# Kernel optimization log

Measured on AMD Instinct MI355X. Metric: run time of the kernel, lower is better.

Reference implementation:

```python
import jax, jax.numpy as jnp
import numpy as np
import math

B, T, F, H = 8, 1024, 1024, 16
D = F // H

def setup_inputs() -> dict:
    key = jax.random.key(0)
    ks = jax.random.split(key, 6)
    s = 1.0 / math.sqrt(F)
    return {
        "qkv": jax.random.normal(ks[0], (B, T, F), dtype=jnp.float32),
        "key_padding_mask": jax.random.randint(ks[1], (B, T), 0, 2).astype(bool),
        "in_proj_w": jax.random.normal(ks[2], (3 * F, F), dtype=jnp.float32) * s,
        "in_proj_b": jax.random.normal(ks[3], (3 * F,), dtype=jnp.float32) * 0.02,
        "out_proj_w": jax.random.normal(ks[4], (F, F), dtype=jnp.float32) * s,
        "out_proj_b": jax.random.normal(ks[5], (F,), dtype=jnp.float32) * 0.02,
    }

def reference(qkv, key_padding_mask, in_proj_w, in_proj_b, out_proj_w, out_proj_b):
    b, t, f = qkv.shape
    h, d = H, f // H
    norm = jnp.asarray(math.sqrt(d), dtype=qkv.dtype)
    # fused QKV projection (torch Linear: x @ W.T + b)
    x = qkv @ in_proj_w.T + in_proj_b                     # [B, T, 3F]
    q, k, v = jnp.split(x, 3, axis=-1)
    q = q.reshape(b, t, h, d).transpose(0, 2, 1, 3)       # [B, H, T, D]
    k = k.reshape(b, t, h, d).transpose(0, 2, 1, 3)
    v = v.reshape(b, t, h, d).transpose(0, 2, 1, 3)
    dot = jnp.einsum("bhqd,bhkd->bhqk", q, k) / norm      # [B, H, T, T]
    dot = jnp.where(key_padding_mask[:, None, None, :], -jnp.inf, dot)
    alpha = jax.nn.softmax(dot, axis=-1)                  # [B, H, T, T]
    att = jnp.einsum("bhqk,bhkd->bhqd", alpha, v)         # [B, H, T, D]
    att = att.transpose(0, 2, 1, 3).reshape(b, t, f)      # [B, T, F]
    out = att @ out_proj_w.T + out_proj_b
    return (out, alpha)
```

## Files before the change

### kernel.cpp

```cpp
#include <hip/hip_runtime.h>
#include <math.h>

#define B_ 8
#define T_ 1024
#define F_ 1024
#define H_ 16
#define D_ 64

typedef __bf16 bf16x8 __attribute__((ext_vector_type(8)));
typedef float f32x4 __attribute__((ext_vector_type(4)));
typedef unsigned short u16x8 __attribute__((ext_vector_type(8)));

__device__ __forceinline__ unsigned short f2bf(float f) {
    union { float f; unsigned u; } v; v.f = f;
    unsigned r = v.u + 0x7fffu + ((v.u >> 16) & 1u);
    return (unsigned short)(r >> 16);
}

__device__ __forceinline__ void gld16(const void* g, void* l) {
    __builtin_amdgcn_global_load_lds(
        (const __attribute__((address_space(1))) void*)g,
        (__attribute__((address_space(3))) void*)l, 16, 0, 0);
}

__device__ __forceinline__ int swz4(int row15) {
    return (row15 ^ (row15 >> 2)) & 3;
}

__global__ __launch_bounds__(256) void cvt_f32_bf16(
    const float* __restrict__ in, unsigned short* __restrict__ out, int n8)
{
    int i = blockIdx.x * 256 + threadIdx.x;
    if (i >= n8) return;
    const float4* p = (const float4*)in + (size_t)i * 2;
    float4 x = p[0], y = p[1];
    u16x8 o;
    o[0] = f2bf(x.x); o[1] = f2bf(x.y); o[2] = f2bf(x.z); o[3] = f2bf(x.w);
    o[4] = f2bf(y.x); o[5] = f2bf(y.y); o[6] = f2bf(y.z); o[7] = f2bf(y.w);
    ((u16x8*)out)[i] = o;
}

__global__ __launch_bounds__(256) void qkv_gemm(
    const unsigned short* __restrict__ A,
    const unsigned short* __restrict__ Bw,
    const float* __restrict__ bias,
    unsigned short* __restrict__ qb,
    unsigned short* __restrict__ kb,
    unsigned short* __restrict__ vb)
{
    __shared__ __align__(16) unsigned short As[128 * 32];
    __shared__ __align__(16) unsigned short Bs[128 * 32];
    const int K = 1024;
    int tid = threadIdx.x;
    int lane = tid & 63, wave = tid >> 6;
    int wr = wave >> 1, wc = wave & 1;
    int m0 = blockIdx.y * 128, n0 = blockIdx.x * 128;
    int col = lane & 15, quad = lane >> 4;
    int sw = swz4(col);
    int rl = lane >> 2;
    int lc = (lane & 3) ^ swz4(rl);

    f32x4 acc[4][4] = {};
    for (int kc = 0; kc < K; kc += 32) {
        __syncthreads();
        #pragma unroll
        for (int l = 0; l < 2; l++) {
            int ia = wave * 2 + l;
            gld16(A  + (size_t)(m0 + ia * 16 + rl) * K + kc + lc * 8, &As[ia * 512]);
            gld16(Bw + (size_t)(n0 + ia * 16 + rl) * K + kc + lc * 8, &Bs[ia * 512]);
        }
        __syncthreads();
        bf16x8 af[4], bg[4];
        #pragma unroll
        for (int mt = 0; mt < 4; mt++)
            af[mt] = *(const bf16x8*)&As[(wr * 64 + mt * 16 + col) * 32 + ((quad ^ sw)) * 8];
        #pragma unroll
        for (int nt = 0; nt < 4; nt++)
            bg[nt] = *(const bf16x8*)&Bs[(wc * 64 + nt * 16 + col) * 32 + ((quad ^ sw)) * 8];
        #pragma unroll
        for (int mt = 0; mt < 4; mt++)
            #pragma unroll
            for (int nt = 0; nt < 4; nt++)
                acc[mt][nt] = __builtin_amdgcn_mfma_f32_16x16x32_bf16(
                    af[mt], bg[nt], acc[mt][nt], 0, 0, 0);
    }
    int which = n0 >> 10;
    #pragma unroll
    for (int nt = 0; nt < 4; nt++) {
        int n = n0 + wc * 64 + nt * 16 + col;
        int hn = (n & 1023) >> 6, d = n & 63;
        float bn = bias[n];
        #pragma unroll
        for (int mt = 0; mt < 4; mt++) {
            #pragma unroll
            for (int r = 0; r < 4; r++) {
                int m = m0 + wr * 64 + mt * 16 + quad * 4 + r;
                int bb = m >> 10, t = m & 1023;
                unsigned short bf = f2bf(acc[mt][nt][r] + bn);
                if (which == 0)
                    qb[(size_t)((bb * H_ + hn) * T_ + t) * D_ + d] = bf;
                else if (which == 1)
                    kb[(size_t)((bb * H_ + hn) * T_ + t) * D_ + d] = bf;
                else
                    vb[(size_t)((bb * H_ + hn) * D_ + d) * T_ + t] = bf;
            }
        }
    }
}

__global__ __launch_bounds__(256) void attn_kernel(
    const unsigned short* __restrict__ qb,
    const unsigned short* __restrict__ kb,
    const int* __restrict__ mask,
    float* __restrict__ alpha)
{
    __shared__ __align__(16) unsigned short Qs[16 * 72];
    __shared__ __align__(16) unsigned short Ks[4][64 * 64];
    __shared__ float redmax[4][16];
    __shared__ float redsum[4][16];
    int b = blockIdx.z, h = blockIdx.y, q0 = blockIdx.x * 16;
    int tid = threadIdx.x, lane = tid & 63, wave = tid >> 6;
    int col = lane & 15, quad = lane >> 4;
    const unsigned short* qbase = qb + ((size_t)(b * H_ + h) * T_ + q0) * D_;
    const unsigned short* kbase = kb + ((size_t)(b * H_ + h) * T_) * D_;

    if (tid < 128) {
        int r = tid >> 3, c = tid & 7;
        *(u16x8*)&Qs[r * 72 + c * 8] = *(const u16x8*)&qbase[r * 64 + c * 8];
    }
    int krl = lane >> 3;
    int klc = (lane & 7) ^ krl;
    int sw8 = col & 7;
    f32x4 acc[4][4] = {};
    bf16x8 aq0, aq1;
    for (int it = 0; it < 4; it++) {
        int kr0 = wave * 256 + it * 64;
        #pragma unroll
        for (int j = 0; j < 8; j++)
            gld16(kbase + (size_t)(kr0 + j * 8 + krl) * 64 + klc * 8, &Ks[wave][j * 512]);
        __syncthreads();
        if (it == 0) {
            aq0 = *(const bf16x8*)&Qs[col * 72 + quad * 8];
            aq1 = *(const bf16x8*)&Qs[col * 72 + 32 + quad * 8];
        }
        #pragma unroll
        for (int ct = 0; ct < 4; ct++) {
            int r = ct * 16 + col;
            const unsigned short* kp = &Ks[wave][r * 64];
            bf16x8 b0 = *(const bf16x8*)&kp[(quad ^ sw8) * 8];
            bf16x8 b1 = *(const bf16x8*)&kp[((4 + quad) ^ sw8) * 8];
            acc[it][ct] = __builtin_amdgcn_mfma_f32_16x16x32_bf16(aq0, b0, acc[it][ct], 0, 0, 0);
            acc[it][ct] = __builtin_amdgcn_mfma_f32_16x16x32_bf16(aq1, b1, acc[it][ct], 0, 0, 0);
        }
        __syncthreads();
    }
    const int* mrow = mask + b * T_;
    float mx[4] = {-INFINITY, -INFINITY, -INFINITY, -INFINITY};
    #pragma unroll
    for (int it = 0; it < 4; it++)
        #pragma unroll
        for (int ct = 0; ct < 4; ct++) {
            int k = wave * 256 + it * 64 + ct * 16 + col;
            bool m = mrow[k] != 0;
            #pragma unroll
            for (int r = 0; r < 4; r++) {
                float v = m ? -INFINITY : acc[it][ct][r] * 0.125f;
                acc[it][ct][r] = v;
                mx[r] = fmaxf(mx[r], v);
            }
        }
    #pragma unroll
    for (int r = 0; r < 4; r++) {
        mx[r] = fmaxf(mx[r], __shfl_xor(mx[r], 1, 64));
        mx[r] = fmaxf(mx[r], __shfl_xor(mx[r], 2, 64));
        mx[r] = fmaxf(mx[r], __shfl_xor(mx[r], 4, 64));
        mx[r] = fmaxf(mx[r], __shfl_xor(mx[r], 8, 64));
    }
    if (col == 0)
        #pragma unroll
        for (int r = 0; r < 4; r++) redmax[wave][quad * 4 + r] = mx[r];
    __syncthreads();
    float gm[4];
    #pragma unroll
    for (int r = 0; r < 4; r++) {
        int row = quad * 4 + r;
        gm[r] = fmaxf(fmaxf(redmax[0][row], redmax[1][row]),
                      fmaxf(redmax[2][row], redmax[3][row]));
    }
    float sm[4] = {0.f, 0.f, 0.f, 0.f};
    #pragma unroll
    for (int it = 0; it < 4; it++)
        #pragma unroll
        for (int ct = 0; ct < 4; ct++)
            #pragma unroll
            for (int r = 0; r < 4; r++) {
                float e = __expf(acc[it][ct][r] - gm[r]);
                acc[it][ct][r] = e;
                sm[r] += e;
            }
    #pragma unroll
    for (int r = 0; r < 4; r++) {
        sm[r] += __shfl_xor(sm[r], 1, 64);
        sm[r] += __shfl_xor(sm[r], 2, 64);
        sm[r] += __shfl_xor(sm[r], 4, 64);
        sm[r] += __shfl_xor(sm[r], 8, 64);
    }
    if (col == 0)
        #pragma unroll
        for (int r = 0; r < 4; r++) redsum[wave][quad * 4 + r] = sm[r];
    __syncthreads();
    float inv[4];
    #pragma unroll
    for (int r = 0; r < 4; r++) {
        int row = quad * 4 + r;
        inv[r] = 1.0f / (redsum[0][row] + redsum[1][row] + redsum[2][row] + redsum[3][row]);
    }
    float* abase = alpha + ((size_t)(b * H_ + h) * T_ + q0) * T_;
    #pragma unroll
    for (int it = 0; it < 4; it++)
        #pragma unroll
        for (int ct = 0; ct < 4; ct++) {
            int k = wave * 256 + it * 64 + ct * 16 + col;
            #pragma unroll
            for (int r = 0; r < 4; r++)
                abase[(size_t)(quad * 4 + r) * T_ + k] = acc[it][ct][r] * inv[r];
        }
}

__global__ __launch_bounds__(256) void attn_v_kernel(
    const float* __restrict__ alpha,
    const unsigned short* __restrict__ vb,
    unsigned short* __restrict__ attb)
{
    __shared__ __align__(16) unsigned short As[64 * 72];
    __shared__ __align__(16) unsigned short Vs[64 * 32];
    int b = blockIdx.z, h = blockIdx.y, q0 = blockIdx.x * 64;
    int tid = threadIdx.x, lane = tid & 63, wave = tid >> 6;
    int col = lane & 15, quad = lane >> 4;
    int swv = swz4(col);
    const float* abase = alpha + ((size_t)(b * H_ + h) * T_ + q0) * T_;
    const unsigned short* vbase = vb + (size_t)(b * H_ + h) * D_ * T_;
    int ar = tid >> 2, acg = tid & 3;
    int vrl = lane >> 2;
    int vlc = (lane & 3) ^ swz4(vrl);
    f32x4 acc[4] = {};
    for (int kc = 0; kc < T_; kc += 32) {
        __syncthreads();
        gld16(vbase + (size_t)(wave * 16 + vrl) * T_ + kc + vlc * 8, &Vs[wave * 512]);
        float4 x = *(const float4*)&abase[(size_t)ar * T_ + kc + acg * 8];
        float4 y = *(const float4*)&abase[(size_t)ar * T_ + kc + acg * 8 + 4];
        u16x8 p;
        p[0] = f2bf(x.x); p[1] = f2bf(x.y); p[2] = f2bf(x.z); p[3] = f2bf(x.w);
        p[4] = f2bf(y.x); p[5] = f2bf(y.y); p[6] = f2bf(y.z); p[7] = f2bf(y.w);
        *(u16x8*)&As[ar * 72 + acg * 8] = p;
        __syncthreads();
        bf16x8 af = *(const bf16x8*)&As[(wave * 16 + col) * 72 + quad * 8];
        #pragma unroll
        for (int nt = 0; nt < 4; nt++) {
            int r = nt * 16 + col;
            bf16x8 bv = *(const bf16x8*)&Vs[r * 32 + ((quad ^ swv)) * 8];
            acc[nt] = __builtin_amdgcn_mfma_f32_16x16x32_bf16(af, bv, acc[nt], 0, 0, 0);
        }
    }
    #pragma unroll
    for (int nt = 0; nt < 4; nt++) {
        int d = nt * 16 + col;
        #pragma unroll
        for (int r = 0; r < 4; r++) {
            int t = q0 + wave * 16 + quad * 4 + r;
            attb[(size_t)(b * T_ + t) * F_ + h * D_ + d] = f2bf(acc[nt][r]);
        }
    }
}

__global__ __launch_bounds__(256) void out_gemm(
    const unsigned short* __restrict__ A,
    const unsigned short* __restrict__ Bw,
    const float* __restrict__ bias,
    float* __restrict__ out)
{
    __shared__ __align__(16) unsigned short As[128 * 32];
    __shared__ __align__(16) unsigned short Bs[128 * 32];
    const int K = 1024;
    int tid = threadIdx.x;
    int lane = tid & 63, wave = tid >> 6;
    int wr = wave >> 1, wc = wave & 1;
    int m0 = blockIdx.y * 128, n0 = blockIdx.x * 128;
    int col = lane & 15, quad = lane >> 4;
    int sw = swz4(col);
    int rl = lane >> 2;
    int lc = (lane & 3) ^ swz4(rl);
    f32x4 acc[4][4] = {};
    for (int kc = 0; kc < K; kc += 32) {
        __syncthreads();
        #pragma unroll
        for (int l = 0; l < 2; l++) {
            int ia = wave * 2 + l;
            gld16(A  + (size_t)(m0 + ia * 16 + rl) * K + kc + lc * 8, &As[ia * 512]);
            gld16(Bw + (size_t)(n0 + ia * 16 + rl) * K + kc + lc * 8, &Bs[ia * 512]);
        }
        __syncthreads();
        bf16x8 af[4], bg[4];
        #pragma unroll
        for (int mt = 0; mt < 4; mt++)
            af[mt] = *(const bf16x8*)&As[(wr * 64 + mt * 16 + col) * 32 + ((quad ^ sw)) * 8];
        #pragma unroll
        for (int nt = 0; nt < 4; nt++)
            bg[nt] = *(const bf16x8*)&Bs[(wc * 64 + nt * 16 + col) * 32 + ((quad ^ sw)) * 8];
        #pragma unroll
        for (int mt = 0; mt < 4; mt++)
            #pragma unroll
            for (int nt = 0; nt < 4; nt++)
                acc[mt][nt] = __builtin_amdgcn_mfma_f32_16x16x32_bf16(
                    af[mt], bg[nt], acc[mt][nt], 0, 0, 0);
    }
    #pragma unroll
    for (int nt = 0; nt < 4; nt++) {
        int n = n0 + wc * 64 + nt * 16 + col;
        float bn = bias[n];
        #pragma unroll
        for (int mt = 0; mt < 4; mt++) {
            #pragma unroll
            for (int r = 0; r < 4; r++) {
                int m = m0 + wr * 64 + mt * 16 + quad * 4 + r;
                out[(size_t)m * F_ + n] = acc[mt][nt][r] + bn;
            }
        }
    }
}

extern "C" void kernel_launch(void* const* d_in, const int* in_sizes, int n_in,
                              void* d_out, int out_size, void* d_ws, size_t ws_size,
                              hipStream_t stream)
{
    const float* qkv   = (const float*)d_in[0];
    const int*   mask  = (const int*)d_in[1];
    const float* in_w  = (const float*)d_in[2];
    const float* in_b  = (const float*)d_in[3];
    const float* out_w = (const float*)d_in[4];
    const float* out_b = (const float*)d_in[5];
    float* out = (float*)d_out;
    const size_t NE = (size_t)B_ * T_ * F_;
    float* alpha = out + NE;

    unsigned short* ws   = (unsigned short*)d_ws;
    unsigned short* Xb   = ws;
    unsigned short* Wib  = Xb  + NE;
    unsigned short* Wob  = Wib + 3 * F_ * F_;
    unsigned short* qb2  = Wob + (size_t)F_ * F_;
    unsigned short* kb2  = qb2 + NE;
    unsigned short* vb2  = kb2 + NE;
    unsigned short* attb = vb2 + NE;

    cvt_f32_bf16<<<dim3((int)(NE / 8 / 256)), 256, 0, stream>>>(qkv, Xb, (int)(NE / 8));
    cvt_f32_bf16<<<dim3(3 * F_ * F_ / 8 / 256), 256, 0, stream>>>(in_w, Wib, 3 * F_ * F_ / 8);
    cvt_f32_bf16<<<dim3(F_ * F_ / 8 / 256), 256, 0, stream>>>(out_w, Wob, F_ * F_ / 8);

    qkv_gemm<<<dim3(24, 64), 256, 0, stream>>>(Xb, Wib, in_b, qb2, kb2, vb2);
    attn_kernel<<<dim3(64, H_, B_), 256, 0, stream>>>(qb2, kb2, mask, alpha);
    attn_v_kernel<<<dim3(16, H_, B_), 256, 0, stream>>>(alpha, vb2, attb);
    out_gemm<<<dim3(8, 64), 256, 0, stream>>>(attb, Wob, out_b, out);
}
```

Baseline: 963.0 us.

## Fuse softmax-probability times V into attention kernel to avoid re-reading alpha

Merges the attention-score/softmax kernel with the alpha·V kernel. Normalized probabilities are kept as bf16 in shared memory, in a buffer that reuses the K staging area, and multiplied by V tiles inside the same block. This removes the second kernel's re-read of the 512MB fp32 alpha tensor from global memory. In exchange it raises LDS usage per block, which may reduce occupancy, and each block now streams all of V for its head instead of sharing V across 64 query rows.

```diff
diff --git a/kernel.cpp b/kernel.cpp
--- a/kernel.cpp
+++ b/kernel.cpp
@@ -108,14 +108,17 @@
     }
 }
 
-__global__ __launch_bounds__(256) void attn_kernel(
+__global__ __launch_bounds__(256) void fused_attn(
     const unsigned short* __restrict__ qb,
     const unsigned short* __restrict__ kb,
+    const unsigned short* __restrict__ vb,
     const int* __restrict__ mask,
-    float* __restrict__ alpha)
-{
+    float* __restrict__ alpha,
+    unsigned short* __restrict__ attb)
+{
+    __shared__ __align__(16) unsigned short U[16 * 1032];
+    __shared__ __align__(16) unsigned short Vs[4][2048];
     __shared__ __align__(16) unsigned short Qs[16 * 72];
-    __shared__ __align__(16) unsigned short Ks[4][64 * 64];
     __shared__ float redmax[4][16];
     __shared__ float redsum[4][16];
     int b = blockIdx.z, h = blockIdx.y, q0 = blockIdx.x * 16;
@@ -123,6 +126,7 @@
     int col = lane & 15, quad = lane >> 4;
     const unsigned short* qbase = qb + ((size_t)(b * H_ + h) * T_ + q0) * D_;
     const unsigned short* kbase = kb + ((size_t)(b * H_ + h) * T_) * D_;
+    unsigned short* Ksw = &U[wave * 4096];
 
     if (tid < 128) {
         int r = tid >> 3, c = tid & 7;
@@ -137,7 +141,7 @@
         int kr0 = wave * 256 + it * 64;
         #pragma unroll
         for (int j = 0; j < 8; j++)
-            gld16(kbase + (size_t)(kr0 + j * 8 + krl) * 64 + klc * 8, &Ks[wave][j * 512]);
+            gld16(kbase + (size_t)(kr0 + j * 8 + krl) * 64 + klc * 8, &Ksw[j * 512]);
         __syncthreads();
         if (it == 0) {
             aq0 = *(const bf16x8*)&Qs[col * 72 + quad * 8];
@@ -146,7 +150,7 @@
         #pragma unroll
         for (int ct = 0; ct < 4; ct++) {
             int r = ct * 16 + col;
-            const unsigned short* kp = &Ks[wave][r * 64];
+            const unsigned short* kp = &Ksw[r * 64];
             bf16x8 b0 = *(const bf16x8*)&kp[(quad ^ sw8) * 8];
             bf16x8 b1 = *(const bf16x8*)&kp[((4 + quad) ^ sw8) * 8];
             acc[it][ct] = __builtin_amdgcn_mfma_f32_16x16x32_bf16(aq0, b0, acc[it][ct], 0, 0, 0);
@@ -222,54 +226,37 @@
         for (int ct = 0; ct < 4; ct++) {
             int k = wave * 256 + it * 64 + ct * 16 + col;
             #pragma unroll
-            for (int r = 0; r < 4; r++)
-                abase[(size_t)(quad * 4 + r) * T_ + k] = acc[it][ct][r] * inv[r];
-        }
-}
-
-__global__ __launch_bounds__(256) void attn_v_kernel(
-    const float* __restrict__ alpha,
-    const unsigned short* __restrict__ vb,
-    unsigned short* __restrict__ attb)
-{
-    __shared__ __align__(16) unsigned short As[64 * 72];
-    __shared__ __align__(16) unsigned short Vs[64 * 32];
-    int b = blockIdx.z, h = blockIdx.y, q0 = blockIdx.x * 64;
-    int tid = threadIdx.x, lane = tid & 63, wave = tid >> 6;
-    int col = lane & 15, quad = lane >> 4;
-    int swv = swz4(col);
-    const float* abase = alpha + ((size_t)(b * H_ + h) * T_ + q0) * T_;
-    const unsigned short* vbase = vb + (size_t)(b * H_ + h) * D_ * T_;
-    int ar = tid >> 2, acg = tid & 3;
-    int vrl = lane >> 2;
-    int vlc = (lane & 3) ^ swz4(vrl);
-    f32x4 acc[4] = {};
-    for (int kc = 0; kc < T_; kc += 32) {
-        __syncthreads();
-        gld16(vbase + (size_t)(wave * 16 + vrl) * T_ + kc + vlc * 8, &Vs[wave * 512]);
-        float4 x = *(const float4*)&abase[(size_t)ar * T_ + kc + acg * 8];
-        float4 y = *(const float4*)&abase[(size_t)ar * T_ + kc + acg * 8 + 4];
-        u16x8 p;
-        p[0] = f2bf(x.x); p[1] = f2bf(x.y); p[2] = f2bf(x.z); p[3] = f2bf(x.w);
-        p[4] = f2bf(y.x); p[5] = f2bf(y.y); p[6] = f2bf(y.z); p[7] = f2bf(y.w);
-        *(u16x8*)&As[ar * 72 + acg * 8] = p;
-        __syncthreads();
-        bf16x8 af = *(const bf16x8*)&As[(wave * 16 + col) * 72 + quad * 8];
-        #pragma unroll
-        for (int nt = 0; nt < 4; nt++) {
-            int r = nt * 16 + col;
-            bf16x8 bv = *(const bf16x8*)&Vs[r * 32 + ((quad ^ swv)) * 8];
-            acc[nt] = __builtin_amdgcn_mfma_f32_16x16x32_bf16(af, bv, acc[nt], 0, 0, 0);
-        }
-    }
-    #pragma unroll
-    for (int nt = 0; nt < 4; nt++) {
-        int d = nt * 16 + col;
-        #pragma unroll
-        for (int r = 0; r < 4; r++) {
-            int t = q0 + wave * 16 + quad * 4 + r;
-            attb[(size_t)(b * T_ + t) * F_ + h * D_ + d] = f2bf(acc[nt][r]);
-        }
+            for (int r = 0; r < 4; r++) {
+                float v = acc[it][ct][r] * inv[r];
+                abase[(size_t)(quad * 4 + r) * T_ + k] = v;
+                U[(quad * 4 + r) * 1032 + k] = f2bf(v);
+            }
+        }
+    __syncthreads();
+    const unsigned short* vhead = vb + (size_t)(b * H_ + h) * D_ * T_;
+    f32x4 oacc = {};
+    for (int kc = 0; kc < T_; kc += 128) {
+        asm volatile("s_waitcnt lgkmcnt(0)" ::: "memory");
+        __builtin_amdgcn_sched_barrier(0);
+        #pragma unroll
+        for (int i = 0; i < 4; i++) {
+            int r = i * 4 + quad;
+            gld16(vhead + (size_t)(wave * 16 + r) * T_ + kc + (col ^ (r & 7)) * 8,
+                  &Vs[wave][i * 512]);
+        }
+        asm volatile("s_waitcnt vmcnt(0)" ::: "memory");
+        __builtin_amdgcn_sched_barrier(0);
+        #pragma unroll
+        for (int w = 0; w < 4; w++) {
+            bf16x8 pa = *(const bf16x8*)&U[col * 1032 + kc + w * 32 + quad * 8];
+            bf16x8 bv = *(const bf16x8*)&Vs[wave][col * 128 + (((w * 4 + quad) ^ (col & 7))) * 8];
+            oacc = __builtin_amdgcn_mfma_f32_16x16x32_bf16(pa, bv, oacc, 0, 0, 0);
+        }
+    }
+    #pragma unroll
+    for (int r = 0; r < 4; r++) {
+        int t = q0 + quad * 4 + r;
+        attb[(size_t)(b * T_ + t) * F_ + h * D_ + wave * 16 + col] = f2bf(oacc[r]);
     }
 }
 
@@ -357,7 +344,6 @@
     cvt_f32_bf16<<<dim3(F_ * F_ / 8 / 256), 256, 0, stream>>>(out_w, Wob, F_ * F_ / 8);
 
     qkv_gemm<<<dim3(24, 64), 256, 0, stream>>>(Xb, Wib, in_b, qb2, kb2, vb2);
-    attn_kernel<<<dim3(64, H_, B_), 256, 0, stream>>>(qb2, kb2, mask, alpha);
-    attn_v_kernel<<<dim3(16, H_, B_), 256, 0, stream>>>(alpha, vb2, attb);
+    fused_attn<<<dim3(64, H_, B_), 256, 0, stream>>>(qb2, kb2, vb2, mask, alpha, attb);
     out_gemm<<<dim3(8, 64), 256, 0, stream>>>(attb, Wob, out_b, out);
 }
```

After: 907.6 us. 1.06x faster.
